# Kernel optimization log

Hardware: AMD Instinct MI355X
Metric: run time of the kernel (lower is better)

The kernel has to match this reference:

```python
import jax, jax.numpy as jnp
import numpy as np

B, C, H, W, HEADS = 16, 512, 64, 64, 8
EPS = 1e-5


def setup_inputs() -> dict:
    key = jax.random.key(0)
    ks = jax.random.split(key, 5)
    s = C ** -0.5  # kaiming-ish scale for 1x1 conv weights
    return {
        "x": jax.random.normal(ks[0], (B, C, H, W), dtype=jnp.float32),
        "Wq": jax.random.normal(ks[1], (C, C), dtype=jnp.float32) * s,
        "Wk": jax.random.normal(ks[2], (C, C), dtype=jnp.float32) * s,
        "Wv": jax.random.normal(ks[3], (C, C), dtype=jnp.float32) * s,
        "Wo": jax.random.normal(ks[4], (C, C), dtype=jnp.float32) * s,
        "gamma": jnp.ones((C,), dtype=jnp.float32),
        "beta": jnp.zeros((C,), dtype=jnp.float32),
    }


def reference(x, Wq, Wk, Wv, Wo, gamma, beta):
    Bb, Cc, Hh, Ww = x.shape
    d = Cc // HEADS  # head_dim
    n = Hh * Ww      # number of spatial positions

    def proj(Wt):
        # 1x1 conv (no bias) == per-position channel matmul
        return jnp.einsum('oc,bchw->bohw', Wt, x).reshape(Bb, HEADS, d, n)

    q = proj(Wq)
    k = proj(Wk)
    v = proj(Wv)

    # softmax over head_dim axis (dim=-2 in the torch code)
    k = jax.nn.softmax(k, axis=-2)

    # linear attention: context = k @ v^T  -> [B, heads, d, d]
    context = jnp.einsum('bhdn,bhen->bhde', k, v)
    # out = (q^T @ context)^T -> [B, heads, d, n]
    out = jnp.einsum('bhdn,bhde->bhen', q, context)

    out = out.reshape(Bb, Cc, Hh, Ww)
    out = jnp.einsum('oc,bchw->bohw', Wo, out)

    y = out + x  # residual

    # BatchNorm2d (training-mode batch statistics, biased variance)
    mean = jnp.mean(y, axis=(0, 2, 3), keepdims=True)
    var = jnp.var(y, axis=(0, 2, 3), keepdims=True)
    yn = (y - mean) * jax.lax.rsqrt(var + EPS)
    return yn * gamma[None, :, None, None] + beta[None, :, None, None]
```

## Files before the change

kernel.cpp:

```cpp
#include <hip/hip_runtime.h>


typedef __bf16 bf16_t;
typedef bf16_t bf16x8 __attribute__((ext_vector_type(8)));
typedef float f32x4 __attribute__((ext_vector_type(4)));
typedef unsigned short u16;

__device__ __forceinline__ u16 f2bf(float f) {
    unsigned u = __builtin_bit_cast(unsigned, f);
    u += 0x7FFFu + ((u >> 16) & 1u);
    return (u16)(u >> 16);
}
__device__ __forceinline__ float bf2f(u16 h) {
    return __builtin_bit_cast(float, ((unsigned)h) << 16);
}

__device__ __forceinline__ void gload_lds16(const u16* g, u16* l) {
    __builtin_amdgcn_global_load_lds((const __attribute__((address_space(1))) void*)g,
                                     (__attribute__((address_space(3))) void*)l, 16, 0, 0);
}
__device__ __forceinline__ bf16x8 ldfrag(const u16* p) {
    return *(const bf16x8*)p;
}

__global__ __launch_bounds__(256) void cast_weights(const float* __restrict__ Wq, const float* __restrict__ Wk,
                                                    const float* __restrict__ Wv, const float* __restrict__ Wo,
                                                    u16* __restrict__ WqT, u16* __restrict__ WkB,
                                                    u16* __restrict__ WvB, u16* __restrict__ WoB) {
    int i = blockIdx.x * 256 + threadIdx.x;
    WkB[i] = f2bf(Wk[i]);
    WvB[i] = f2bf(Wv[i]);
    WoB[i] = f2bf(Wo[i]);
    int o = i >> 9, c = i & 511;
    WqT[c * 512 + o] = f2bf(Wq[i]);
}

__global__ __launch_bounds__(256) void transpose_cast(const float* __restrict__ x, u16* __restrict__ xT) {
    __shared__ u16 tile[64][65];
    int nt = blockIdx.x, ct = blockIdx.y, b = blockIdx.z;
    const float* xb = x + ((size_t)b * 512 + ct * 64) * 4096 + nt * 64;
    int t = threadIdx.x;
#pragma unroll
    for (int i = 0; i < 16; ++i) {
        int idx = i * 256 + t;
        int cl = idx >> 6, nl = idx & 63;
        tile[cl][nl] = f2bf(xb[(size_t)cl * 4096 + nl]);
    }
    __syncthreads();
    u16* xTb = xT + ((size_t)b * 4096 + nt * 64) * 512 + ct * 64;
#pragma unroll
    for (int i = 0; i < 16; ++i) {
        int idx = i * 256 + t;
        int nl = idx >> 6, cl = idx & 63;
        xTb[(size_t)nl * 512 + cl] = tile[cl][nl];
    }
}

__device__ __forceinline__ void gemm128_dbuf(const u16* __restrict__ Ab, const u16* __restrict__ Btb,
                                             u16* lds, f32x4 acc[4][4]) {
    const int t = threadIdx.x;
    const int l = t & 63, w = t >> 6;
    const int lrow = l & 15, lk = l >> 4;
    const int wm = w >> 1, wn = w & 1;
    const int r0 = t & 127, k40 = t >> 7;
    gload_lds16(Ab + (size_t)r0 * 512 + k40 * 8, lds + t * 8);
    gload_lds16(Ab + (size_t)r0 * 512 + (k40 + 2) * 8, lds + (t + 256) * 8);
    gload_lds16(Btb + (size_t)r0 * 512 + k40 * 8, lds + 4096 + t * 8);
    gload_lds16(Btb + (size_t)r0 * 512 + (k40 + 2) * 8, lds + 4096 + (t + 256) * 8);
    __syncthreads();
    for (int kt = 0; kt < 16; ++kt) {
        const int cur = (kt & 1) << 13;
        const int nxt = cur ^ 8192;
        if (kt < 15) {
            const int kb = (kt + 1) * 32;
            gload_lds16(Ab + (size_t)r0 * 512 + kb + k40 * 8, lds + nxt + t * 8);
            gload_lds16(Ab + (size_t)r0 * 512 + kb + (k40 + 2) * 8, lds + nxt + (t + 256) * 8);
            gload_lds16(Btb + (size_t)r0 * 512 + kb + k40 * 8, lds + nxt + 4096 + t * 8);
            gload_lds16(Btb + (size_t)r0 * 512 + kb + (k40 + 2) * 8, lds + nxt + 4096 + (t + 256) * 8);
        }
        bf16x8 av[4], bv[4];
#pragma unroll
        for (int fi = 0; fi < 4; ++fi)
            av[fi] = ldfrag(lds + cur + lk * 1024 + (wm * 64 + fi * 16 + lrow) * 8);
#pragma unroll
        for (int fj = 0; fj < 4; ++fj)
            bv[fj] = ldfrag(lds + cur + 4096 + lk * 1024 + (wn * 64 + fj * 16 + lrow) * 8);
#pragma unroll
        for (int fi = 0; fi < 4; ++fi)
#pragma unroll
            for (int fj = 0; fj < 4; ++fj)
                acc[fi][fj] = __builtin_amdgcn_mfma_f32_16x16x32_bf16(av[fi], bv[fj], acc[fi][fj], 0, 0, 0);
        __syncthreads();
    }
}

__global__ __launch_bounds__(256) void kgemm_kv(const u16* __restrict__ Wkv, const u16* __restrict__ xT,
                                                u16* __restrict__ K, u16* __restrict__ V) {
    __shared__ __align__(16) u16 lds[16384];
    const int b = blockIdx.y;
    const int bm = blockIdx.x >> 5, bn = blockIdx.x & 31;
    const u16* Ab = Wkv + (size_t)bm * 128 * 512;
    const u16* Btb = xT + (size_t)b * 2097152 + (size_t)bn * 128 * 512;
    f32x4 acc[4][4];
#pragma unroll
    for (int i = 0; i < 4; ++i)
#pragma unroll
        for (int j = 0; j < 4; ++j) acc[i][j] = (f32x4){0.f, 0.f, 0.f, 0.f};
    gemm128_dbuf(Ab, Btb, lds, acc);
    const int t = threadIdx.x, l = t & 63, w = t >> 6;
    const int lrow = l & 15, lk = l >> 4;
    const int wm = w >> 1, wn = w & 1;
    u16* Cb = (bm < 4) ? (K + (size_t)b * 2097152 + (size_t)bm * 128 * 4096)
                       : (V + (size_t)b * 2097152 + (size_t)(bm - 4) * 128 * 4096);
#pragma unroll
    for (int fi = 0; fi < 4; ++fi)
#pragma unroll
        for (int fj = 0; fj < 4; ++fj)
#pragma unroll
            for (int r = 0; r < 4; ++r) {
                int m = wm * 64 + fi * 16 + lk * 4 + r;
                int n = bn * 128 + wn * 64 + fj * 16 + lrow;
                Cb[(size_t)m * 4096 + n] = f2bf(acc[fi][fj][r]);
            }
}

__global__ __launch_bounds__(256) void kgemm_bf16(const u16* __restrict__ A, long long sA,
                                                  const u16* __restrict__ Bt, long long sB,
                                                  u16* __restrict__ C, long long sC, int ldc, int Nt) {
    __shared__ __align__(16) u16 lds[16384];
    const int b = blockIdx.y;
    const int bm = blockIdx.x / Nt, bn = blockIdx.x % Nt;
    const u16* Ab = A + (size_t)b * sA + (size_t)bm * 128 * 512;
    const u16* Btb = Bt + (size_t)b * sB + (size_t)bn * 128 * 512;
    f32x4 acc[4][4];
#pragma unroll
    for (int i = 0; i < 4; ++i)
#pragma unroll
        for (int j = 0; j < 4; ++j) acc[i][j] = (f32x4){0.f, 0.f, 0.f, 0.f};
    gemm128_dbuf(Ab, Btb, lds, acc);
    const int t = threadIdx.x, l = t & 63, w = t >> 6;
    const int lrow = l & 15, lk = l >> 4;
    const int wm = w >> 1, wn = w & 1;
    u16* Cb = C + (size_t)b * sC;
#pragma unroll
    for (int fi = 0; fi < 4; ++fi)
#pragma unroll
        for (int fj = 0; fj < 4; ++fj)
#pragma unroll
            for (int r = 0; r < 4; ++r) {
                int m = bm * 128 + wm * 64 + fi * 16 + lk * 4 + r;
                int n = bn * 128 + wn * 64 + fj * 16 + lrow;
                Cb[(size_t)m * ldc + n] = f2bf(acc[fi][fj][r]);
            }
}

__global__ __launch_bounds__(256) void kgemm_f32res(const u16* __restrict__ Wfin, const u16* __restrict__ xT,
                                                    const float* __restrict__ xres, u16* __restrict__ yb,
                                                    float* __restrict__ sums, float* __restrict__ sumsq) {
    __shared__ __align__(16) u16 lds[16384];
    const int b = blockIdx.y;
    const int bm = blockIdx.x >> 5, bn = blockIdx.x & 31;
    const u16* Ab = Wfin + (size_t)b * 262144 + (size_t)bm * 128 * 512;
    const u16* Btb = xT + (size_t)b * 2097152 + (size_t)bn * 128 * 512;
    f32x4 acc[4][4];
#pragma unroll
    for (int i = 0; i < 4; ++i)
#pragma unroll
        for (int j = 0; j < 4; ++j) acc[i][j] = (f32x4){0.f, 0.f, 0.f, 0.f};
    gemm128_dbuf(Ab, Btb, lds, acc);
    const int t = threadIdx.x, l = t & 63, w = t >> 6;
    const int lrow = l & 15, lk = l >> 4;
    const int wm = w >> 1, wn = w & 1;
#pragma unroll
    for (int fi = 0; fi < 4; ++fi)
#pragma unroll
        for (int r = 0; r < 4; ++r) {
            int mg = bm * 128 + wm * 64 + fi * 16 + lk * 4 + r;
            size_t rowbase = (size_t)b * 2097152 + (size_t)mg * 4096 + bn * 128 + wn * 64;
            float rs = 0.f, rq = 0.f;
#pragma unroll
            for (int fj = 0; fj < 4; ++fj) {
                int nc = fj * 16 + lrow;
                float v = acc[fi][fj][r] + xres[rowbase + nc];
                yb[rowbase + nc] = f2bf(v);
                rs += v; rq += v * v;
            }
#pragma unroll
            for (int off = 1; off < 16; off <<= 1) {
                rs += __shfl_xor(rs, off);
                rq += __shfl_xor(rq, off);
            }
            if (lrow == 0) {
                atomicAdd(&sums[mg], rs);
                atomicAdd(&sumsq[mg], rq);
            }
        }
}

__global__ __launch_bounds__(256) void softmax_k(u16* __restrict__ K) {
    int gid = blockIdx.x * 256 + threadIdx.x;
    int n = gid & 4095, bh = gid >> 12;
    u16* p = K + (size_t)bh * 64 * 4096 + n;
    float v[64];
    float m = -1e30f;
#pragma unroll
    for (int d = 0; d < 64; ++d) { v[d] = bf2f(p[(size_t)d * 4096]); m = fmaxf(m, v[d]); }
    float s = 0.f;
#pragma unroll
    for (int d = 0; d < 64; ++d) { v[d] = __expf(v[d] - m); s += v[d]; }
    float inv = 1.0f / s;
#pragma unroll
    for (int d = 0; d < 64; ++d) p[(size_t)d * 4096] = f2bf(v[d] * inv);
}

__global__ __launch_bounds__(256) void ctx_partial(const u16* __restrict__ Ksm, const u16* __restrict__ V,
                                                   float* __restrict__ P) {
    __shared__ __align__(16) u16 lds[8192];
    const int bh = blockIdx.x >> 3, ks = blockIdx.x & 7;
    const u16* Ab = Ksm + (size_t)bh * 262144;
    const u16* Btb = V + (size_t)bh * 262144;
    const int t = threadIdx.x, l = t & 63, w = t >> 6;
    const int lrow = l & 15, lk = l >> 4;
    const int wm = w >> 1, wn = w & 1;
    const int row = t & 63, k4 = t >> 6;
    f32x4 acc[2][2];
#pragma unroll
    for (int i = 0; i < 2; ++i)
#pragma unroll
        for (int j = 0; j < 2; ++j) acc[i][j] = (f32x4){0.f, 0.f, 0.f, 0.f};
    gload_lds16(Ab + (size_t)row * 4096 + ks * 512 + k4 * 8, lds + t * 8);
    gload_lds16(Btb + (size_t)row * 4096 + ks * 512 + k4 * 8, lds + 2048 + t * 8);
    __syncthreads();
    for (int kt = 0; kt < 16; ++kt) {
        const int cur = (kt & 1) << 12;
        const int nxt = cur ^ 4096;
        if (kt < 15) {
            const int kb = ks * 512 + (kt + 1) * 32;
            gload_lds16(Ab + (size_t)row * 4096 + kb + k4 * 8, lds + nxt + t * 8);
            gload_lds16(Btb + (size_t)row * 4096 + kb + k4 * 8, lds + nxt + 2048 + t * 8);
        }
        bf16x8 av[2], bv[2];
#pragma unroll
        for (int fi = 0; fi < 2; ++fi)
            av[fi] = ldfrag(lds + cur + lk * 512 + (wm * 32 + fi * 16 + lrow) * 8);
#pragma unroll
        for (int fj = 0; fj < 2; ++fj)
            bv[fj] = ldfrag(lds + cur + 2048 + lk * 512 + (wn * 32 + fj * 16 + lrow) * 8);
#pragma unroll
        for (int fi = 0; fi < 2; ++fi)
#pragma unroll
            for (int fj = 0; fj < 2; ++fj)
                acc[fi][fj] = __builtin_amdgcn_mfma_f32_16x16x32_bf16(av[fi], bv[fj], acc[fi][fj], 0, 0, 0);
        __syncthreads();
    }
    float* Pb = P + (size_t)blockIdx.x * 4096;
#pragma unroll
    for (int fi = 0; fi < 2; ++fi)
#pragma unroll
        for (int fj = 0; fj < 2; ++fj)
#pragma unroll
            for (int r = 0; r < 4; ++r) {
                int m = wm * 32 + fi * 16 + lk * 4 + r;
                int e = wn * 32 + fj * 16 + lrow;
                Pb[m * 64 + e] = acc[fi][fj][r];
            }
}

__global__ __launch_bounds__(256) void ctx_reduce(const float* __restrict__ P, u16* __restrict__ ctxT) {
    int gid = blockIdx.x * 256 + threadIdx.x;
    int d = gid & 63, e = (gid >> 6) & 63, bh = gid >> 12;
    const float* p = P + (size_t)bh * 8 * 4096 + d * 64 + e;
    float s = 0.f;
#pragma unroll
    for (int ks = 0; ks < 8; ++ks) s += p[(size_t)ks * 4096];
    ctxT[(size_t)bh * 4096 + e * 64 + d] = f2bf(s);
}

__global__ __launch_bounds__(256) void kgemm_wqp(const u16* __restrict__ ctxT, const u16* __restrict__ WqT,
                                                 u16* __restrict__ WqpT) {
    __shared__ __align__(16) u16 lds[4096 + 8192];
    const int nq = blockIdx.x, bh = blockIdx.y;
    const int b = bh >> 3, h = bh & 7;
    const u16* Ab = ctxT + (size_t)bh * 4096;
    const u16* Btb = WqT + (size_t)nq * 128 * 512 + h * 64;
    u16* Asl = lds; u16* Bsl = lds + 4096;
    const int t = threadIdx.x, l = t & 63, w = t >> 6;
    const int lrow = l & 15, lk = l >> 4;
    {
        int q = t;
        gload_lds16(Ab + (size_t)(q & 63) * 64 + (q >> 6) * 8, Asl + q * 8);
        q = t + 256;
        gload_lds16(Ab + (size_t)(q & 63) * 64 + (q >> 6) * 8, Asl + q * 8);
    }
#pragma unroll
    for (int i = 0; i < 4; ++i) {
        int q = t + i * 256;
        gload_lds16(Btb + (size_t)(q & 127) * 512 + (q >> 7) * 8, Bsl + q * 8);
    }
    __syncthreads();
    f32x4 acc[4][2];
#pragma unroll
    for (int i = 0; i < 4; ++i)
#pragma unroll
        for (int j = 0; j < 2; ++j) acc[i][j] = (f32x4){0.f, 0.f, 0.f, 0.f};
#pragma unroll
    for (int ksv = 0; ksv < 2; ++ksv) {
        bf16x8 av[4], bv[2];
#pragma unroll
        for (int fi = 0; fi < 4; ++fi)
            av[fi] = ldfrag(Asl + (ksv * 4 + lk) * 512 + (fi * 16 + lrow) * 8);
#pragma unroll
        for (int fj = 0; fj < 2; ++fj)
            bv[fj] = ldfrag(Bsl + (ksv * 4 + lk) * 1024 + (w * 32 + fj * 16 + lrow) * 8);
#pragma unroll
        for (int fi = 0; fi < 4; ++fi)
#pragma unroll
            for (int fj = 0; fj < 2; ++fj)
                acc[fi][fj] = __builtin_amdgcn_mfma_f32_16x16x32_bf16(av[fi], bv[fj], acc[fi][fj], 0, 0, 0);
    }
    u16* Ob = WqpT + (size_t)b * 262144 + h * 64;
#pragma unroll
    for (int fi = 0; fi < 4; ++fi)
#pragma unroll
        for (int fj = 0; fj < 2; ++fj)
#pragma unroll
            for (int r = 0; r < 4; ++r) {
                int e = fi * 16 + lk * 4 + r;
                int c = nq * 128 + w * 32 + fj * 16 + lrow;
                Ob[(size_t)c * 512 + e] = f2bf(acc[fi][fj][r]);
            }
}

__global__ void bn_finalize(const float* __restrict__ sums, const float* __restrict__ sumsq,
                            const float* __restrict__ gamma, const float* __restrict__ beta,
                            float* __restrict__ scale, float* __restrict__ shift) {
    int c = threadIdx.x;
    float inv = 1.0f / 65536.0f;
    float mean = sums[c] * inv;
    float var = sumsq[c] * inv - mean * mean;
    float rstd = rsqrtf(var + 1e-5f);
    float sc = rstd * gamma[c];
    scale[c] = sc;
    shift[c] = beta[c] - mean * sc;
}

__global__ __launch_bounds__(256) void bn_norm(const u16* __restrict__ yb, const float* __restrict__ scale,
                                               const float* __restrict__ shift, float* __restrict__ out) {
    int i8 = blockIdx.x * 256 + threadIdx.x;
    uint4 raw = ((const uint4*)yb)[i8];
    int c = (i8 >> 9) & 511;
    float sc = scale[c], sh = shift[c];
    float4 o0, o1;
    o0.x = bf2f((u16)(raw.x & 0xffff)) * sc + sh;  o0.y = bf2f((u16)(raw.x >> 16)) * sc + sh;
    o0.z = bf2f((u16)(raw.y & 0xffff)) * sc + sh;  o0.w = bf2f((u16)(raw.y >> 16)) * sc + sh;
    o1.x = bf2f((u16)(raw.z & 0xffff)) * sc + sh;  o1.y = bf2f((u16)(raw.z >> 16)) * sc + sh;
    o1.z = bf2f((u16)(raw.w & 0xffff)) * sc + sh;  o1.w = bf2f((u16)(raw.w >> 16)) * sc + sh;
    float4* O = (float4*)out;
    O[(size_t)i8 * 2] = o0;
    O[(size_t)i8 * 2 + 1] = o1;
}

extern "C" void kernel_launch(void* const* d_in, const int* in_sizes, int n_in,
                              void* d_out, int out_size, void* d_ws, size_t ws_size,
                              hipStream_t stream) {
    const float* x     = (const float*)d_in[0];
    const float* Wq    = (const float*)d_in[1];
    const float* Wk    = (const float*)d_in[2];
    const float* Wv    = (const float*)d_in[3];
    const float* Wo    = (const float*)d_in[4];
    const float* gamma = (const float*)d_in[5];
    const float* beta  = (const float*)d_in[6];

    char* w = (char*)d_ws;
    u16* xT   = (u16*)(w);
    u16* Kbuf = (u16*)(w + 67108864ull);
    u16* WqT  = (u16*)(w + 134217728ull);
    u16* WkB  = WqT + 262144;
    u16* WvB  = WkB + 262144;
    u16* WoB  = WvB + 262144;
    u16* Wfin = WoB + 262144;
    float* sums  = (float*)(w + 134217728ull + 2097152ull + 8388608ull);
    float* sumsq = sums + 512;
    float* scale = sums + 1024;
    float* shift = sums + 1536;
    u16* ybuf = Kbuf;

    char* ob = (char*)d_out;
    float* ctxP = (float*)ob;
    u16* Vbuf   = (u16*)(ob + 16777216ull);
    u16* ctxT   = (u16*)(ob + 83886080ull);
    u16* WqpT   = (u16*)(ob + 84934656ull);
    float* out  = (float*)d_out;

    hipMemsetAsync(sums, 0, 4096, stream);
    cast_weights<<<1024, 256, 0, stream>>>(Wq, Wk, Wv, Wo, WqT, WkB, WvB, WoB);
    transpose_cast<<<dim3(64, 8, 16), 256, 0, stream>>>(x, xT);
    kgemm_kv<<<dim3(256, 16), 256, 0, stream>>>(WkB, xT, Kbuf, Vbuf);
    softmax_k<<<2048, 256, 0, stream>>>(Kbuf);
    ctx_partial<<<1024, 256, 0, stream>>>(Kbuf, Vbuf, ctxP);
    ctx_reduce<<<2048, 256, 0, stream>>>(ctxP, ctxT);
    kgemm_wqp<<<dim3(4, 128), 256, 0, stream>>>(ctxT, WqT, WqpT);
    kgemm_bf16<<<dim3(16, 16), 256, 0, stream>>>(WoB, 0, WqpT, 262144, Wfin, 262144, 512, 4);
    kgemm_f32res<<<dim3(128, 16), 256, 0, stream>>>(Wfin, xT, x, ybuf, sums, sumsq);
    bn_finalize<<<1, 512, 0, stream>>>(sums, sumsq, gamma, beta, scale, shift);
    bn_norm<<<16384, 256, 0, stream>>>(ybuf, scale, shift, out);
}
```

Baseline: 675.9 us.

## Replace double-buffered GEMM staging with three-stage LDS ring and explicit vmcnt waits

The GEMM mainloops (shared 128x128 GEMM and ctx_partial) move from a two-buffer LDS scheme to a three-buffer ring that prefetches two k-tiles ahead. __syncthreads is replaced by explicit s_waitcnt vmcnt counts and raw s_barrier, so only the oldest tile's loads are waited on. The loop is also fully unrolled. This raises LDS usage by half per block, which may lower occupancy, and the hand-written waitcnt counts must exactly match the number of outstanding loads per stage.

Measured after the change: 653.2 us. 1.03x faster.

```diff
diff --git a/kernel.cpp b/kernel.cpp
--- a/kernel.cpp
+++ b/kernel.cpp
@@ -5,6 +5,9 @@
 typedef bf16_t bf16x8 __attribute__((ext_vector_type(8)));
 typedef float f32x4 __attribute__((ext_vector_type(4)));
 typedef unsigned short u16;
+
+#define VMWAIT(N) asm volatile("s_waitcnt vmcnt(" #N ")" ::: "memory")
+#define SBAR()    asm volatile("s_barrier" ::: "memory")
 
 __device__ __forceinline__ u16 f2bf(float f) {
     unsigned u = __builtin_bit_cast(unsigned, f);
@@ -56,47 +59,54 @@
     }
 }
 
-__device__ __forceinline__ void gemm128_dbuf(const u16* __restrict__ Ab, const u16* __restrict__ Btb,
+__device__ __forceinline__ void stageAB128(const u16* __restrict__ Ab, const u16* __restrict__ Btb,
+                                           u16* base, int kb, int t) {
+    const int r0 = t & 127, k40 = t >> 7;
+    gload_lds16(Ab + (size_t)r0 * 512 + kb + k40 * 8, base + t * 8);
+    gload_lds16(Ab + (size_t)r0 * 512 + kb + (k40 + 2) * 8, base + (t + 256) * 8);
+    gload_lds16(Btb + (size_t)r0 * 512 + kb + k40 * 8, base + 4096 + t * 8);
+    gload_lds16(Btb + (size_t)r0 * 512 + kb + (k40 + 2) * 8, base + 4096 + (t + 256) * 8);
+}
+
+__device__ __forceinline__ void gemm128_ring(const u16* __restrict__ Ab, const u16* __restrict__ Btb,
                                              u16* lds, f32x4 acc[4][4]) {
     const int t = threadIdx.x;
     const int l = t & 63, w = t >> 6;
     const int lrow = l & 15, lk = l >> 4;
     const int wm = w >> 1, wn = w & 1;
-    const int r0 = t & 127, k40 = t >> 7;
-    gload_lds16(Ab + (size_t)r0 * 512 + k40 * 8, lds + t * 8);
-    gload_lds16(Ab + (size_t)r0 * 512 + (k40 + 2) * 8, lds + (t + 256) * 8);
-    gload_lds16(Btb + (size_t)r0 * 512 + k40 * 8, lds + 4096 + t * 8);
-    gload_lds16(Btb + (size_t)r0 * 512 + (k40 + 2) * 8, lds + 4096 + (t + 256) * 8);
-    __syncthreads();
+    stageAB128(Ab, Btb, lds, 0, t);
+    stageAB128(Ab, Btb, lds + 8192, 32, t);
+#pragma unroll
     for (int kt = 0; kt < 16; ++kt) {
-        const int cur = (kt & 1) << 13;
-        const int nxt = cur ^ 8192;
-        if (kt < 15) {
-            const int kb = (kt + 1) * 32;
-            gload_lds16(Ab + (size_t)r0 * 512 + kb + k40 * 8, lds + nxt + t * 8);
-            gload_lds16(Ab + (size_t)r0 * 512 + kb + (k40 + 2) * 8, lds + nxt + (t + 256) * 8);
-            gload_lds16(Btb + (size_t)r0 * 512 + kb + k40 * 8, lds + nxt + 4096 + t * 8);
-            gload_lds16(Btb + (size_t)r0 * 512 + kb + (k40 + 2) * 8, lds + nxt + 4096 + (t + 256) * 8);
+        u16* cur = lds + (kt % 3) * 8192;
+        if (kt < 14) {
+            stageAB128(Ab, Btb, lds + ((kt + 2) % 3) * 8192, (kt + 2) * 32, t);
+            VMWAIT(8);
+        } else if (kt == 14) {
+            VMWAIT(4);
+        } else {
+            VMWAIT(0);
         }
+        SBAR();
         bf16x8 av[4], bv[4];
 #pragma unroll
         for (int fi = 0; fi < 4; ++fi)
-            av[fi] = ldfrag(lds + cur + lk * 1024 + (wm * 64 + fi * 16 + lrow) * 8);
+            av[fi] = ldfrag(cur + lk * 1024 + (wm * 64 + fi * 16 + lrow) * 8);
 #pragma unroll
         for (int fj = 0; fj < 4; ++fj)
-            bv[fj] = ldfrag(lds + cur + 4096 + lk * 1024 + (wn * 64 + fj * 16 + lrow) * 8);
+            bv[fj] = ldfrag(cur + 4096 + lk * 1024 + (wn * 64 + fj * 16 + lrow) * 8);
 #pragma unroll
         for (int fi = 0; fi < 4; ++fi)
 #pragma unroll
             for (int fj = 0; fj < 4; ++fj)
                 acc[fi][fj] = __builtin_amdgcn_mfma_f32_16x16x32_bf16(av[fi], bv[fj], acc[fi][fj], 0, 0, 0);
-        __syncthreads();
+        SBAR();
     }
 }
 
 __global__ __launch_bounds__(256) void kgemm_kv(const u16* __restrict__ Wkv, const u16* __restrict__ xT,
                                                 u16* __restrict__ K, u16* __restrict__ V) {
-    __shared__ __align__(16) u16 lds[16384];
+    __shared__ __align__(16) u16 lds[24576];
     const int b = blockIdx.y;
     const int bm = blockIdx.x >> 5, bn = blockIdx.x & 31;
     const u16* Ab = Wkv + (size_t)bm * 128 * 512;
@@ -106,7 +116,7 @@
     for (int i = 0; i < 4; ++i)
 #pragma unroll
         for (int j = 0; j < 4; ++j) acc[i][j] = (f32x4){0.f, 0.f, 0.f, 0.f};
-    gemm128_dbuf(Ab, Btb, lds, acc);
+    gemm128_ring(Ab, Btb, lds, acc);
     const int t = threadIdx.x, l = t & 63, w = t >> 6;
     const int lrow = l & 15, lk = l >> 4;
     const int wm = w >> 1, wn = w & 1;
@@ -127,7 +137,7 @@
 __global__ __launch_bounds__(256) void kgemm_bf16(const u16* __restrict__ A, long long sA,
                                                   const u16* __restrict__ Bt, long long sB,
                                                   u16* __restrict__ C, long long sC, int ldc, int Nt) {
-    __shared__ __align__(16) u16 lds[16384];
+    __shared__ __align__(16) u16 lds[24576];
     const int b = blockIdx.y;
     const int bm = blockIdx.x / Nt, bn = blockIdx.x % Nt;
     const u16* Ab = A + (size_t)b * sA + (size_t)bm * 128 * 512;
@@ -137,7 +147,7 @@
     for (int i = 0; i < 4; ++i)
 #pragma unroll
         for (int j = 0; j < 4; ++j) acc[i][j] = (f32x4){0.f, 0.f, 0.f, 0.f};
-    gemm128_dbuf(Ab, Btb, lds, acc);
+    gemm128_ring(Ab, Btb, lds, acc);
     const int t = threadIdx.x, l = t & 63, w = t >> 6;
     const int lrow = l & 15, lk = l >> 4;
     const int wm = w >> 1, wn = w & 1;
@@ -157,7 +167,7 @@
 __global__ __launch_bounds__(256) void kgemm_f32res(const u16* __restrict__ Wfin, const u16* __restrict__ xT,
                                                     const float* __restrict__ xres, u16* __restrict__ yb,
                                                     float* __restrict__ sums, float* __restrict__ sumsq) {
-    __shared__ __align__(16) u16 lds[16384];
+    __shared__ __align__(16) u16 lds[24576];
     const int b = blockIdx.y;
     const int bm = blockIdx.x >> 5, bn = blockIdx.x & 31;
     const u16* Ab = Wfin + (size_t)b * 262144 + (size_t)bm * 128 * 512;
@@ -167,7 +177,7 @@
     for (int i = 0; i < 4; ++i)
 #pragma unroll
         for (int j = 0; j < 4; ++j) acc[i][j] = (f32x4){0.f, 0.f, 0.f, 0.f};
-    gemm128_dbuf(Ab, Btb, lds, acc);
+    gemm128_ring(Ab, Btb, lds, acc);
     const int t = threadIdx.x, l = t & 63, w = t >> 6;
     const int lrow = l & 15, lk = l >> 4;
     const int wm = w >> 1, wn = w & 1;
@@ -215,7 +225,7 @@
 
 __global__ __launch_bounds__(256) void ctx_partial(const u16* __restrict__ Ksm, const u16* __restrict__ V,
                                                    float* __restrict__ P) {
-    __shared__ __align__(16) u16 lds[8192];
+    __shared__ __align__(16) u16 lds[12288];
     const int bh = blockIdx.x >> 3, ks = blockIdx.x & 7;
     const u16* Ab = Ksm + (size_t)bh * 262144;
     const u16* Btb = V + (size_t)bh * 262144;
@@ -228,30 +238,38 @@
     for (int i = 0; i < 2; ++i)
 #pragma unroll
         for (int j = 0; j < 2; ++j) acc[i][j] = (f32x4){0.f, 0.f, 0.f, 0.f};
-    gload_lds16(Ab + (size_t)row * 4096 + ks * 512 + k4 * 8, lds + t * 8);
-    gload_lds16(Btb + (size_t)row * 4096 + ks * 512 + k4 * 8, lds + 2048 + t * 8);
-    __syncthreads();
+    const size_t rA = (size_t)row * 4096 + ks * 512 + k4 * 8;
+    gload_lds16(Ab + rA, lds + t * 8);
+    gload_lds16(Btb + rA, lds + 2048 + t * 8);
+    gload_lds16(Ab + rA + 32, lds + 4096 + t * 8);
+    gload_lds16(Btb + rA + 32, lds + 6144 + t * 8);
+#pragma unroll
     for (int kt = 0; kt < 16; ++kt) {
-        const int cur = (kt & 1) << 12;
-        const int nxt = cur ^ 4096;
-        if (kt < 15) {
-            const int kb = ks * 512 + (kt + 1) * 32;
-            gload_lds16(Ab + (size_t)row * 4096 + kb + k4 * 8, lds + nxt + t * 8);
-            gload_lds16(Btb + (size_t)row * 4096 + kb + k4 * 8, lds + nxt + 2048 + t * 8);
+        u16* cur = lds + (kt % 3) * 4096;
+        if (kt < 14) {
+            u16* nb = lds + ((kt + 2) % 3) * 4096;
+            gload_lds16(Ab + rA + (kt + 2) * 32, nb + t * 8);
+            gload_lds16(Btb + rA + (kt + 2) * 32, nb + 2048 + t * 8);
+            VMWAIT(4);
+        } else if (kt == 14) {
+            VMWAIT(2);
+        } else {
+            VMWAIT(0);
         }
+        SBAR();
         bf16x8 av[2], bv[2];
 #pragma unroll
         for (int fi = 0; fi < 2; ++fi)
-            av[fi] = ldfrag(lds + cur + lk * 512 + (wm * 32 + fi * 16 + lrow) * 8);
+            av[fi] = ldfrag(cur + lk * 512 + (wm * 32 + fi * 16 + lrow) * 8);
 #pragma unroll
         for (int fj = 0; fj < 2; ++fj)
-            bv[fj] = ldfrag(lds + cur + 2048 + lk * 512 + (wn * 32 + fj * 16 + lrow) * 8);
+            bv[fj] = ldfrag(cur + 2048 + lk * 512 + (wn * 32 + fj * 16 + lrow) * 8);
 #pragma unroll
         for (int fi = 0; fi < 2; ++fi)
 #pragma unroll
             for (int fj = 0; fj < 2; ++fj)
                 acc[fi][fj] = __builtin_amdgcn_mfma_f32_16x16x32_bf16(av[fi], bv[fj], acc[fi][fj], 0, 0, 0);
-        __syncthreads();
+        SBAR();
     }
     float* Pb = P + (size_t)blockIdx.x * 4096;
 #pragma unroll
```
